# Optimization experiments

Hardware: AMD Instinct MI355X
Metric: run time of the kernel (lower is better)

Reference implementation:

```python
import jax, jax.numpy as jnp
import numpy as np
import math

B, S, H, NH, NKV = 4, 2048, 2048, 16, 8
HD = H // NH           # 128
N_REP = NH // NKV      # 2


def rotate_half(t):
    t1, t2 = jnp.split(t, 2, axis=-1)
    return jnp.concatenate([-t2, t1], axis=-1)


def setup_inputs() -> dict:
    key = jax.random.key(0)
    ks = jax.random.split(key, 6)
    x = jax.random.normal(ks[0], (B, S, H), dtype=jnp.float32)
    # realistic RoPE tables [max_pos, head_dim]
    inv_freq = 1.0 / (10000.0 ** (np.arange(0, HD, 2, dtype=np.float32) / HD))
    t = np.arange(S, dtype=np.float32)
    freqs = np.outer(t, inv_freq)                 # [S, HD/2]
    emb = np.concatenate([freqs, freqs], axis=-1)  # [S, HD]
    cos = jnp.asarray(np.cos(emb), dtype=jnp.float32)
    sin = jnp.asarray(np.sin(emb), dtype=jnp.float32)
    sc = 0.02
    Wq = jax.random.normal(ks[1], (H, NH * HD), dtype=jnp.float32) * sc
    Wk = jax.random.normal(ks[2], (H, NKV * HD), dtype=jnp.float32) * sc
    Wv = jax.random.normal(ks[3], (H, NKV * HD), dtype=jnp.float32) * sc
    Wo = jax.random.normal(ks[4], (NH * HD, H), dtype=jnp.float32) * sc
    return {"x": x, "cos": cos, "sin": sin, "Wq": Wq, "Wk": Wk, "Wv": Wv, "Wo": Wo}


def reference(x, cos, sin, Wq, Wk, Wv, Wo):
    bsz, seq_len, _ = x.shape
    xq = (x @ Wq).reshape(bsz, seq_len, NH, HD)
    xk = (x @ Wk).reshape(bsz, seq_len, NKV, HD)
    xv = (x @ Wv).reshape(bsz, seq_len, NKV, HD)

    # RoPE (past_len = 0, no cache)
    c = cos[:seq_len][None, :, None, :]   # [1,S,1,HD]
    s = sin[:seq_len][None, :, None, :]
    xq = xq * c + rotate_half(xq) * s
    xk = xk * c + rotate_half(xk) * s

    # repeat_kv (GQA): [B,S,NKV,HD] -> [B,S,NH,HD]
    xk = jnp.repeat(xk, N_REP, axis=2)
    xv = jnp.repeat(xv, N_REP, axis=2)

    q = xq.transpose(0, 2, 1, 3)  # [B,NH,S,HD]
    k = xk.transpose(0, 2, 1, 3)
    v = xv.transpose(0, 2, 1, 3)

    scores = jnp.einsum('bhqd,bhkd->bhqk', q, k) / math.sqrt(HD)
    causal = jnp.triu(jnp.full((seq_len, seq_len), -jnp.inf, dtype=scores.dtype), k=1)
    scores = scores + causal[None, None]
    probs = jax.nn.softmax(scores.astype(jnp.float32), axis=-1).astype(q.dtype)
    out = jnp.einsum('bhqk,bhkd->bhqd', probs, v)
    out = out.transpose(0, 2, 1, 3).reshape(bsz, seq_len, NH * HD)
    return out @ Wo
```

## Files before the change

kernel.cpp:

```cpp
#include <hip/hip_runtime.h>
#include <stdint.h>

using bf16   = __bf16;
using bf16x4 = __attribute__((ext_vector_type(4))) __bf16;
using bf16x8 = __attribute__((ext_vector_type(8))) __bf16;
using f32x4  = __attribute__((ext_vector_type(4))) float;

#define DEV_INLINE __device__ __forceinline__

DEV_INLINE void gload16(const void* g, const void* l) {
  __builtin_amdgcn_global_load_lds(
      (const __attribute__((address_space(1))) unsigned int*)(uintptr_t)g,
      (__attribute__((address_space(3))) unsigned int*)(unsigned int)(uintptr_t)l,
      16, 0, 0);
}

DEV_INLINE f32x4 mfma16(bf16x8 a, bf16x8 b, f32x4 c) {
  return __builtin_amdgcn_mfma_f32_16x16x32_bf16(a, b, c, 0, 0, 0);
}

__global__ void cast_f32_bf16(const float4* __restrict__ in, bf16* __restrict__ out, int n4) {
  int i = blockIdx.x * 256 + threadIdx.x;
  if (i >= n4) return;
  float4 v = in[i];
  bf16x4 o = { (bf16)v.x, (bf16)v.y, (bf16)v.z, (bf16)v.w };
  *(bf16x4*)(out + (size_t)i * 4) = o;
}

__global__ void transpose_cast(const float* __restrict__ in, bf16* __restrict__ out,
                               int rows, int cols) {
  __shared__ float tile[32][33];
  int c0 = blockIdx.x * 32, r0 = blockIdx.y * 32;
  int t = threadIdx.x, tc = t & 31, tr = t >> 5;
  for (int i = 0; i < 4; ++i)
    tile[tr + i*8][tc] = in[(size_t)(r0 + tr + i*8) * cols + (c0 + tc)];
  __syncthreads();
  for (int i = 0; i < 4; ++i)
    out[(size_t)(c0 + tr + i*8) * rows + (r0 + tc)] = (bf16)tile[tc][tr + i*8];
}


DEV_INLINE void stage_half(const bf16* __restrict__ src, int K, int k0, bf16* slot,
                           int w, int lr, int lc) {
#pragma unroll
  for (int i = 0; i < 2; ++i)
    gload16(src + (size_t)(w*16 + lr) * K + (k0 + i*32 + lc*8), slot + (w*2 + i) * 512);
}

DEV_INLINE void load_afr(bf16x8 (&af)[4][2], const bf16* slot, int wr2, int l) {
#pragma unroll
  for (int mi = 0; mi < 4; ++mi)
#pragma unroll
    for (int ks = 0; ks < 2; ++ks)
      af[mi][ks] = *(const bf16x8*)(slot + ((wr2*4 + mi)*2 + ks) * 512 + l*8);
}

template<bool PERM>
DEV_INLINE void load_bfr(bf16x8 (&bfr)[2][2], const bf16* slot, int wc2, int l) {
#pragma unroll
  for (int ni = 0; ni < 2; ++ni)
#pragma unroll
    for (int ks = 0; ks < 2; ++ks) {
      int mt = PERM ? (ni*4 + wc2) : (wc2*2 + ni);
      bfr[ni][ks] = *(const bf16x8*)(slot + (mt*2 + ks) * 512 + l*8);
    }
}

DEV_INLINE void mfma_quad(f32x4 (&aq)[4][2], const bf16x8 (&af)[4][2],
                          const bf16x8 (&bfr)[2][2]) {
#pragma unroll
  for (int mi = 0; mi < 4; ++mi)
#pragma unroll
    for (int ni = 0; ni < 2; ++ni)
#pragma unroll
      for (int ks = 0; ks < 2; ++ks)
        aq[mi][ni] = mfma16(af[mi][ks], bfr[ni][ks], aq[mi][ni]);
}

#define WAIT_LGKM0() do { \
  asm volatile("s_waitcnt lgkmcnt(0)" ::: "memory"); \
  __builtin_amdgcn_sched_barrier(0); } while (0)

template<bool PERM, int K, int NK>
DEV_INLINE void gemm256_core(const bf16* __restrict__ A, const bf16* __restrict__ Bt,
                             int bm0, int bn0, bf16* sA, bf16* sB,
                             int w, int l, int lr, int lc, int wr2, int wc2,
                             f32x4 (&acc)[2][2][4][2]) {
  const bf16* Ar0 = A  + (size_t)bm0 * K;
  const bf16* Ar1 = Ar0 + (size_t)128 * K;
  const bf16* Br0 = Bt + (size_t)bn0 * K;
  const bf16* Br1 = Br0 + (size_t)128 * K;
  stage_half(Ar0, K, 0,  sA + 0*8192, w, lr, lc);
  stage_half(Br1, K, 0,  sB + 1*8192, w, lr, lc);
  stage_half(Ar1, K, 0,  sA + 1*8192, w, lr, lc);
  stage_half(Br0, K, 0,  sB + 0*8192, w, lr, lc);
  stage_half(Ar0, K, 64, sA + 2*8192, w, lr, lc);
  stage_half(Br1, K, 64, sB + 3*8192, w, lr, lc);
  __syncthreads();

  for (int kt = 0; kt < NK; ++kt) {
    const int k1 = (kt + 1 < NK ? kt + 1 : 0) * 64;
    const int k2 = (kt + 2 < NK ? kt + 2 : 0) * 64;
    bf16* A0s = sA + ((2*kt    ) & 3) * 8192;
    bf16* A1s = sA + ((2*kt + 1) & 3) * 8192;
    bf16* B0s = sB + ((2*kt    ) & 3) * 8192;
    bf16* B1s = sB + ((2*kt + 1) & 3) * 8192;
    bf16x8 af[4][2], bfr[2][2];

    load_afr(af, A0s, wr2, l);
    load_bfr<PERM>(bfr, B0s, wc2, l);
    stage_half(Ar1, K, k1, sA + ((2*kt + 3) & 3) * 8192, w, lr, lc);
    __builtin_amdgcn_s_barrier();
    WAIT_LGKM0();
    __builtin_amdgcn_s_setprio(1);
    mfma_quad(acc[0][0], af, bfr);
    __builtin_amdgcn_s_setprio(0);
    __builtin_amdgcn_s_barrier();

    load_bfr<PERM>(bfr, B1s, wc2, l);
    stage_half(Br0, K, k1, sB + ((2*kt + 2) & 3) * 8192, w, lr, lc);
    __builtin_amdgcn_s_barrier();
    WAIT_LGKM0();
    __builtin_amdgcn_s_setprio(1);
    mfma_quad(acc[0][1], af, bfr);
    __builtin_amdgcn_s_setprio(0);
    __builtin_amdgcn_s_barrier();

    load_afr(af, A1s, wr2, l);
    stage_half(Ar0, K, k2, sA + ((2*kt + 4) & 3) * 8192, w, lr, lc);
    __builtin_amdgcn_s_barrier();
    WAIT_LGKM0();
    __builtin_amdgcn_s_setprio(1);
    mfma_quad(acc[1][1], af, bfr);
    __builtin_amdgcn_s_setprio(0);
    __builtin_amdgcn_s_barrier();

    load_bfr<PERM>(bfr, B0s, wc2, l);
    stage_half(Br1, K, k2, sB + ((2*kt + 5) & 3) * 8192, w, lr, lc);
    __builtin_amdgcn_s_barrier();
    WAIT_LGKM0();
    __builtin_amdgcn_s_setprio(1);
    mfma_quad(acc[1][0], af, bfr);
    __builtin_amdgcn_s_setprio(0);
    asm volatile("s_waitcnt vmcnt(4)" ::: "memory");
    __builtin_amdgcn_sched_barrier(0);
    __builtin_amdgcn_s_barrier();
  }
  asm volatile("s_waitcnt vmcnt(0)" ::: "memory");
}

__global__ __launch_bounds__(512, 2)
void gemm256_rope(const bf16* __restrict__ A, const bf16* __restrict__ Bt,
                  const float* __restrict__ cs, const float* __restrict__ sn,
                  bf16* __restrict__ Qr, bf16* __restrict__ Kr,
                  bf16* __restrict__ Vbuf) {
  __shared__ bf16 sA[4 * 8192];
  __shared__ bf16 sB[4 * 8192];
  int id = blockIdx.x;
  int swz = (id & 7) * 64 + (id >> 3);
  int tm = swz >> 4, tn = swz & 15;
  int bm0 = tm * 256, bn0 = tn * 256;
  int tid = threadIdx.x, w = tid >> 6, l = tid & 63, lr = l & 15, lc = l >> 4;
  int wr2 = w >> 2, wc2 = w & 3;
  f32x4 acc[2][2][4][2] = {};
  gemm256_core<true, 2048, 32>(A, Bt, bm0, bn0, sA, sB, w, l, lr, lc, wr2, wc2, acc);

  int bb = bm0 >> 11, s0 = bm0 & 2047;
  int dlo = wc2 * 16 + lr;
#pragma unroll
  for (int nh = 0; nh < 2; ++nh) {
    int h128 = tn * 2 + nh;
    if (h128 < 24) {
      const float scale = (h128 < 16) ? 0.08838834764831845f * 1.4426950408889634f : 1.0f;
      bf16* dstB = (h128 < 16)
          ? Qr + (size_t)(bb * 16 + h128) * 2048 * 128
          : Kr + (size_t)(bb * 8 + (h128 - 16)) * 2048 * 128;
#pragma unroll
      for (int mh = 0; mh < 2; ++mh)
#pragma unroll
        for (int mi = 0; mi < 4; ++mi)
#pragma unroll
          for (int r = 0; r < 4; ++r) {
            int sl = s0 + mh*128 + wr2*64 + mi*16 + lc*4 + r;
            float c  = cs[sl * 128 + dlo];
            float sv = sn[sl * 128 + dlo];
            float lo = acc[mh][nh][mi][0][r], hi = acc[mh][nh][mi][1][r];
            bf16* dst = dstB + (size_t)sl * 128 + dlo;
            dst[0]  = (bf16)((lo * c - hi * sv) * scale);
            dst[64] = (bf16)((hi * c + lo * sv) * scale);
          }
    } else {
      int kvh = h128 - 24;
#pragma unroll
      for (int mh = 0; mh < 2; ++mh)
#pragma unroll
        for (int mi = 0; mi < 4; ++mi)
#pragma unroll
          for (int r = 0; r < 4; ++r) {
            int sl = s0 + mh*128 + wr2*64 + mi*16 + lc*4 + r;
            bf16* dst = Vbuf + ((size_t)(bb * 2048) + sl) * 1024 + kvh * 128 + dlo;
            dst[0]  = (bf16)acc[mh][nh][mi][0][r];
            dst[64] = (bf16)acc[mh][nh][mi][1][r];
          }
    }
  }
}

__global__ __launch_bounds__(512, 2)
void gemm256_out(const bf16* __restrict__ A, const bf16* __restrict__ Bt,
                 float* __restrict__ C) {
  __shared__ bf16 sA[4 * 8192];
  __shared__ bf16 sB[4 * 8192];
  int id = blockIdx.x;
  int swz = (id & 7) * 32 + (id >> 3);
  int tm = swz >> 3, tn = swz & 7;
  int bm0 = tm * 256, bn0 = tn * 256;
  int tid = threadIdx.x, w = tid >> 6, l = tid & 63, lr = l & 15, lc = l >> 4;
  int wr2 = w >> 2, wc2 = w & 3;
  f32x4 acc[2][2][4][2] = {};
  gemm256_core<false, 2048, 32>(A, Bt, bm0, bn0, sA, sB, w, l, lr, lc, wr2, wc2, acc);
#pragma unroll
  for (int mh = 0; mh < 2; ++mh)
#pragma unroll
    for (int nh = 0; nh < 2; ++nh)
#pragma unroll
      for (int mi = 0; mi < 4; ++mi)
#pragma unroll
        for (int ni = 0; ni < 2; ++ni)
#pragma unroll
          for (int r = 0; r < 4; ++r) {
            int row = bm0 + mh*128 + wr2*64 + mi*16 + lc*4 + r;
            int col = bn0 + nh*128 + wc2*32 + ni*16 + lr;
            C[(size_t)row * 2048 + col] = acc[mh][nh][mi][ni][r];
          }
}

__global__ void v_transpose(const bf16* __restrict__ Vbuf, bf16* __restrict__ Vt) {
  __shared__ bf16 tile[32][33];
  int s0 = blockIdx.x * 32, d0 = blockIdx.y * 32, bh = blockIdx.z;
  int b = bh >> 3, h = bh & 7;
  int t = threadIdx.x, tc = t & 31, tr = t >> 5;
  for (int i = 0; i < 4; ++i)
    tile[tr + i*8][tc] =
        Vbuf[((size_t)(b*2048) + s0 + tr + i*8) * 1024 + h*128 + d0 + tc];
  __syncthreads();
  for (int i = 0; i < 4; ++i)
    Vt[((size_t)bh * 128 + d0 + tr + i*8) * 2048 + s0 + tc] = tile[tc][tr + i*8];
}

__global__ __launch_bounds__(256, 2)
void attn_kernel(const bf16* __restrict__ Q, const bf16* __restrict__ Kg,
                 const bf16* __restrict__ Vt, bf16* __restrict__ Og) {
  __shared__ bf16 sK[32 * 512];
  __shared__ bf16 sV[32 * 512];
  int qi = 31 - blockIdx.x;
  int bkv = blockIdx.y;
  int b = bkv >> 3, kvh = bkv & 7;
  int tid = threadIdx.x, w = tid >> 6, l = tid & 63, lr = l & 15, lc = l >> 4;
  const bf16* Qb0 = Q + ((size_t)(b*16 + kvh*2) * 2048 + qi*64) * 128;
  const bf16* Qb1 = Qb0 + (size_t)2048 * 128;
  const bf16* Kb  = Kg + (size_t)bkv * 2048 * 128;
  const bf16* Vb  = Vt + (size_t)bkv * 128 * 2048;
  bf16x8 qf0[4], qf1[4];
  for (int ks = 0; ks < 4; ++ks) {
    size_t off = (size_t)(w*16 + lr) * 128 + ks*32 + lc*8;
    qf0[ks] = *(const bf16x8*)(Qb0 + off);
    qf1[ks] = *(const bf16x8*)(Qb1 + off);
  }
  f32x4 o0[8] = {}, o1[8] = {};
  float l0[4] = {0.f,0.f,0.f,0.f}, l1[4] = {0.f,0.f,0.f,0.f};
  int qrow = qi*64 + w*16 + lc*4;
  bf16* sP0 = sK + w * 2048;
  bf16* sP1 = sK + 8192 + w * 2048;
  int tmax = (qi + 2) >> 1;
  for (int t = 0; t < tmax; ++t) {
    __syncthreads();
    for (int i = 0; i < 8; ++i) {
      int id = w*8 + i;
      int nt = id >> 2, ks = id & 3;
      gload16(Kb + (size_t)(t*128 + nt*16 + lr) * 128 + ks*32 + lc*8, sK + id*512);
      gload16(Vb + (size_t)(nt*16 + lr) * 2048 + t*128 + ks*32 + lc*8, sV + id*512);
    }
    __syncthreads();
    f32x4 s0[8] = {}, s1[8] = {};
    for (int nt = 0; nt < 8; ++nt)
      for (int ks = 0; ks < 4; ++ks) {
        bf16x8 kf = *(const bf16x8*)(sK + (nt*4 + ks)*512 + l*8);
        s0[nt] = mfma16(qf0[ks], kf, s0[nt]);
        s1[nt] = mfma16(qf1[ks], kf, s1[nt]);
      }
    if (t == tmax - 1) {
      for (int nt = 0; nt < 8; ++nt) {
        int col = t*128 + nt*16 + lr;
        for (int r = 0; r < 4; ++r)
          if (col > qrow + r) { s0[nt][r] = -1e30f; s1[nt][r] = -1e30f; }
      }
    }
    __syncthreads();
    for (int nt = 0; nt < 8; ++nt) {
      int hi6 = (nt >> 2) * 1024;
      int blk = (nt*2 + (lr >> 3)) & 7;
      int off = lr & 7;
      for (int r = 0; r < 4; ++r) {
        int q = lc*4 + r;
        int addr = hi6 + q*64 + ((blk ^ (q & 7)) * 8) + off;
        float p0 = __builtin_amdgcn_exp2f(s0[nt][r]);
        float p1 = __builtin_amdgcn_exp2f(s1[nt][r]);
        l0[r] += p0;
        l1[r] += p1;
        sP0[addr] = (bf16)p0;
        sP1[addr] = (bf16)p1;
      }
    }
    asm volatile("s_waitcnt lgkmcnt(0)" ::: "memory");
    __builtin_amdgcn_sched_barrier(0);
    bf16x8 pf0[4], pf1[4];
    for (int ks = 0; ks < 4; ++ks) {
      int ra = (ks >> 1)*1024 + lr*64 + ((((ks & 1)*4 + lc) ^ (lr & 7)) * 8);
      pf0[ks] = *(const bf16x8*)(sP0 + ra);
      pf1[ks] = *(const bf16x8*)(sP1 + ra);
    }
    for (int nt = 0; nt < 8; ++nt)
      for (int ks = 0; ks < 4; ++ks) {
        bf16x8 vf = *(const bf16x8*)(sV + (nt*4 + ks)*512 + l*8);
        o0[nt] = mfma16(pf0[ks], vf, o0[nt]);
        o1[nt] = mfma16(pf1[ks], vf, o1[nt]);
      }
  }
  for (int msk = 1; msk < 16; msk <<= 1)
    for (int r = 0; r < 4; ++r) {
      l0[r] += __shfl_xor(l0[r], msk, 64);
      l1[r] += __shfl_xor(l1[r], msk, 64);
    }
  for (int r = 0; r < 4; ++r) {
    float inv0 = 1.f / l0[r];
    float inv1 = 1.f / l1[r];
    size_t row = (size_t)(b*2048) + qi*64 + w*16 + lc*4 + r;
    size_t base0 = row * 2048 + (kvh*2) * 128;
    for (int nt = 0; nt < 8; ++nt) {
      Og[base0 + nt*16 + lr]       = (bf16)(o0[nt][r] * inv0);
      Og[base0 + 128 + nt*16 + lr] = (bf16)(o1[nt][r] * inv1);
    }
  }
}

extern "C" void kernel_launch(void* const* d_in, const int* in_sizes, int n_in,
                              void* d_out, int out_size, void* d_ws, size_t ws_size,
                              hipStream_t stream) {
  (void)in_sizes; (void)n_in; (void)out_size; (void)ws_size;
  const float* x  = (const float*)d_in[0];
  const float* cs = (const float*)d_in[1];
  const float* sn = (const float*)d_in[2];
  const float* Wq = (const float*)d_in[3];
  const float* Wk = (const float*)d_in[4];
  const float* Wv = (const float*)d_in[5];
  const float* Wo = (const float*)d_in[6];
  float* out = (float*)d_out;

  char* p = (char*)d_ws;
  bf16* xb    = (bf16*)p;  p += (size_t)8192*2048*2;
  bf16* Wt    = (bf16*)p;  p += (size_t)4096*2048*2;
  bf16* Wot   = (bf16*)p;  p += (size_t)2048*2048*2;
  bf16* Qr    = (bf16*)p;  p += (size_t)64*2048*128*2;
  bf16* Kr    = (bf16*)p;  p += (size_t)32*2048*128*2;
  bf16* Vbuf  = (bf16*)p;  p += (size_t)8192*1024*2;
  bf16* Vtb   = (bf16*)p;  p += (size_t)32*2048*128*2;
  bf16* attnb = (bf16*)p;  p += (size_t)8192*2048*2;

  cast_f32_bf16<<<4194304/256, 256, 0, stream>>>((const float4*)x, xb, 4194304);
  transpose_cast<<<dim3(64,64), 256, 0, stream>>>(Wq, Wt, 2048, 2048);
  transpose_cast<<<dim3(32,64), 256, 0, stream>>>(Wk, Wt + (size_t)2048*2048, 2048, 1024);
  transpose_cast<<<dim3(32,64), 256, 0, stream>>>(Wv, Wt + (size_t)3072*2048, 2048, 1024);
  transpose_cast<<<dim3(64,64), 256, 0, stream>>>(Wo, Wot, 2048, 2048);
  gemm256_rope<<<dim3(512), 512, 0, stream>>>(xb, Wt, cs, sn, Qr, Kr, Vbuf);
  v_transpose<<<dim3(64,4,32), 256, 0, stream>>>(Vbuf, Vtb);
  attn_kernel<<<dim3(32,32), 256, 0, stream>>>(Qr, Kr, Vtb, attnb);
  gemm256_out<<<dim3(256), 512, 0, stream>>>(attnb, Wot, out);
}
```

Baseline: 560.3 us.

## Double-buffer K/V tiles in attention kernel and rotate query-block mapping

The attention kernel now keeps two LDS buffers for K and V and prefetches the next tile with async global-to-LDS loads while the current tile is computed, waiting on vmcnt instead of a full barrier. This hides global load latency behind the QK and PV MFMAs. Q-block indices are also rotated per batch-head so causal work is spread across the grid rather than running longest blocks first. LDS use doubles, which may lower occupancy, and the last iteration issues a redundant reload.

```diff
diff --git a/kernel.cpp b/kernel.cpp
--- a/kernel.cpp
+++ b/kernel.cpp
@@ -18,6 +18,15 @@
 DEV_INLINE f32x4 mfma16(bf16x8 a, bf16x8 b, f32x4 c) {
   return __builtin_amdgcn_mfma_f32_16x16x32_bf16(a, b, c, 0, 0, 0);
 }
+
+#define FENCED_BARRIER() do { \
+  __builtin_amdgcn_sched_barrier(0); \
+  __builtin_amdgcn_s_barrier(); \
+  __builtin_amdgcn_sched_barrier(0); } while (0)
+
+#define WAIT_LGKM0() do { \
+  asm volatile("s_waitcnt lgkmcnt(0)" ::: "memory"); \
+  __builtin_amdgcn_sched_barrier(0); } while (0)
 
 __global__ void cast_f32_bf16(const float4* __restrict__ in, bf16* __restrict__ out, int n4) {
   int i = blockIdx.x * 256 + threadIdx.x;
@@ -76,10 +85,6 @@
       for (int ks = 0; ks < 2; ++ks)
         aq[mi][ni] = mfma16(af[mi][ks], bfr[ni][ks], aq[mi][ni]);
 }
-
-#define WAIT_LGKM0() do { \
-  asm volatile("s_waitcnt lgkmcnt(0)" ::: "memory"); \
-  __builtin_amdgcn_sched_barrier(0); } while (0)
 
 template<bool PERM, int K, int NK>
 DEV_INLINE void gemm256_core(const bf16* __restrict__ A, const bf16* __restrict__ Bt,
@@ -251,10 +256,11 @@
 __global__ __launch_bounds__(256, 2)
 void attn_kernel(const bf16* __restrict__ Q, const bf16* __restrict__ Kg,
                  const bf16* __restrict__ Vt, bf16* __restrict__ Og) {
-  __shared__ bf16 sK[32 * 512];
-  __shared__ bf16 sV[32 * 512];
-  int qi = 31 - blockIdx.x;
-  int bkv = blockIdx.y;
+  __shared__ bf16 sK[2][32 * 512];
+  __shared__ bf16 sV[2][32 * 512];
+  int x = blockIdx.x, y = blockIdx.y;
+  int qi = (x + y) & 31;
+  int bkv = y;
   int b = bkv >> 3, kvh = bkv & 7;
   int tid = threadIdx.x, w = tid >> 6, l = tid & 63, lr = l & 15, lc = l >> 4;
   const bf16* Qb0 = Q + ((size_t)(b*16 + kvh*2) * 2048 + qi*64) * 128;
@@ -270,22 +276,35 @@
   f32x4 o0[8] = {}, o1[8] = {};
   float l0[4] = {0.f,0.f,0.f,0.f}, l1[4] = {0.f,0.f,0.f,0.f};
   int qrow = qi*64 + w*16 + lc*4;
-  bf16* sP0 = sK + w * 2048;
-  bf16* sP1 = sK + 8192 + w * 2048;
   int tmax = (qi + 2) >> 1;
+
+  for (int i = 0; i < 8; ++i) {
+    int id = w*8 + i;
+    int nt = id >> 2, ks = id & 3;
+    gload16(Kb + (size_t)(nt*16 + lr) * 128 + ks*32 + lc*8, sK[0] + id*512);
+    gload16(Vb + (size_t)(nt*16 + lr) * 2048 + ks*32 + lc*8, sV[0] + id*512);
+  }
+
   for (int t = 0; t < tmax; ++t) {
-    __syncthreads();
+    int cur = t & 1;
+    bf16* sKc = sK[cur];
+    bf16* sVc = sV[cur];
+    FENCED_BARRIER();
+    int tc = (t + 1 < tmax) ? t + 1 : t;
     for (int i = 0; i < 8; ++i) {
       int id = w*8 + i;
       int nt = id >> 2, ks = id & 3;
-      gload16(Kb + (size_t)(t*128 + nt*16 + lr) * 128 + ks*32 + lc*8, sK + id*512);
-      gload16(Vb + (size_t)(nt*16 + lr) * 2048 + t*128 + ks*32 + lc*8, sV + id*512);
-    }
-    __syncthreads();
+      gload16(Kb + (size_t)(tc*128 + nt*16 + lr) * 128 + ks*32 + lc*8,
+              sK[cur ^ 1] + id*512);
+      gload16(Vb + (size_t)(nt*16 + lr) * 2048 + tc*128 + ks*32 + lc*8,
+              sV[cur ^ 1] + id*512);
+    }
+    asm volatile("s_waitcnt vmcnt(16)" ::: "memory");
+    FENCED_BARRIER();
     f32x4 s0[8] = {}, s1[8] = {};
     for (int nt = 0; nt < 8; ++nt)
       for (int ks = 0; ks < 4; ++ks) {
-        bf16x8 kf = *(const bf16x8*)(sK + (nt*4 + ks)*512 + l*8);
+        bf16x8 kf = *(const bf16x8*)(sKc + (nt*4 + ks)*512 + l*8);
         s0[nt] = mfma16(qf0[ks], kf, s0[nt]);
         s1[nt] = mfma16(qf1[ks], kf, s1[nt]);
       }
@@ -296,7 +315,10 @@
           if (col > qrow + r) { s0[nt][r] = -1e30f; s1[nt][r] = -1e30f; }
       }
     }
-    __syncthreads();
+    WAIT_LGKM0();
+    FENCED_BARRIER();
+    bf16* sP0 = sKc + w * 2048;
+    bf16* sP1 = sKc + 8192 + w * 2048;
     for (int nt = 0; nt < 8; ++nt) {
       int hi6 = (nt >> 2) * 1024;
       int blk = (nt*2 + (lr >> 3)) & 7;
@@ -312,8 +334,7 @@
         sP1[addr] = (bf16)p1;
       }
     }
-    asm volatile("s_waitcnt lgkmcnt(0)" ::: "memory");
-    __builtin_amdgcn_sched_barrier(0);
+    WAIT_LGKM0();
     bf16x8 pf0[4], pf1[4];
     for (int ks = 0; ks < 4; ++ks) {
       int ra = (ks >> 1)*1024 + lr*64 + ((((ks & 1)*4 + lc) ^ (lr & 7)) * 8);
@@ -322,11 +343,12 @@
     }
     for (int nt = 0; nt < 8; ++nt)
       for (int ks = 0; ks < 4; ++ks) {
-        bf16x8 vf = *(const bf16x8*)(sV + (nt*4 + ks)*512 + l*8);
+        bf16x8 vf = *(const bf16x8*)(sVc + (nt*4 + ks)*512 + l*8);
         o0[nt] = mfma16(pf0[ks], vf, o0[nt]);
         o1[nt] = mfma16(pf1[ks], vf, o1[nt]);
       }
   }
+  asm volatile("s_waitcnt vmcnt(0)" ::: "memory");
   for (int msk = 1; msk < 16; msk <<= 1)
     for (int r = 0; r < 4; ++r) {
       l0[r] += __shfl_xor(l0[r], msk, 64);
```

Measured after the change: 632.5 us. 12.9% more time.

## Shrink attention KV tile to 64 with dedicated P buffer and higher occupancy

Applied to the files above, without the earlier changes.

The attention kernel now processes 64-key tiles instead of 128, which makes the causal tail finer-grained. It gives P its own shared buffer so the sync before the P writes can be removed, and the smaller LDS footprint allows launch bounds of 3 blocks per CU. Query tiles are assigned through a rotated (x+y)&31 mapping to balance causal work across blocks. The trade-off is more loop iterations and barriers per block, plus tighter register limits at occupancy 3.

```diff
diff --git a/kernel.cpp b/kernel.cpp
--- a/kernel.cpp
+++ b/kernel.cpp
@@ -18,6 +18,10 @@
 DEV_INLINE f32x4 mfma16(bf16x8 a, bf16x8 b, f32x4 c) {
   return __builtin_amdgcn_mfma_f32_16x16x32_bf16(a, b, c, 0, 0, 0);
 }
+
+#define WAIT_LGKM0() do { \
+  asm volatile("s_waitcnt lgkmcnt(0)" ::: "memory"); \
+  __builtin_amdgcn_sched_barrier(0); } while (0)
 
 __global__ void cast_f32_bf16(const float4* __restrict__ in, bf16* __restrict__ out, int n4) {
   int i = blockIdx.x * 256 + threadIdx.x;
@@ -76,10 +80,6 @@
       for (int ks = 0; ks < 2; ++ks)
         aq[mi][ni] = mfma16(af[mi][ks], bfr[ni][ks], aq[mi][ni]);
 }
-
-#define WAIT_LGKM0() do { \
-  asm volatile("s_waitcnt lgkmcnt(0)" ::: "memory"); \
-  __builtin_amdgcn_sched_barrier(0); } while (0)
 
 template<bool PERM, int K, int NK>
 DEV_INLINE void gemm256_core(const bf16* __restrict__ A, const bf16* __restrict__ Bt,
@@ -248,13 +248,15 @@
     Vt[((size_t)bh * 128 + d0 + tr + i*8) * 2048 + s0 + tc] = tile[tc][tr + i*8];
 }
 
-__global__ __launch_bounds__(256, 2)
+__global__ __launch_bounds__(256, 3)
 void attn_kernel(const bf16* __restrict__ Q, const bf16* __restrict__ Kg,
                  const bf16* __restrict__ Vt, bf16* __restrict__ Og) {
-  __shared__ bf16 sK[32 * 512];
-  __shared__ bf16 sV[32 * 512];
-  int qi = 31 - blockIdx.x;
-  int bkv = blockIdx.y;
+  __shared__ bf16 sK[16 * 512];
+  __shared__ bf16 sV[16 * 512];
+  __shared__ bf16 sP[8 * 1024];
+  int x = blockIdx.x, y = blockIdx.y;
+  int qi = (x + y) & 31;
+  int bkv = y;
   int b = bkv >> 3, kvh = bkv & 7;
   int tid = threadIdx.x, w = tid >> 6, l = tid & 63, lr = l & 15, lc = l >> 4;
   const bf16* Qb0 = Q + ((size_t)(b*16 + kvh*2) * 2048 + qi*64) * 128;
@@ -270,40 +272,39 @@
   f32x4 o0[8] = {}, o1[8] = {};
   float l0[4] = {0.f,0.f,0.f,0.f}, l1[4] = {0.f,0.f,0.f,0.f};
   int qrow = qi*64 + w*16 + lc*4;
-  bf16* sP0 = sK + w * 2048;
-  bf16* sP1 = sK + 8192 + w * 2048;
-  int tmax = (qi + 2) >> 1;
+  bf16* sP0 = sP + w * 1024;
+  bf16* sP1 = sP + 4096 + w * 1024;
+  int tmax = qi + 1;
   for (int t = 0; t < tmax; ++t) {
     __syncthreads();
-    for (int i = 0; i < 8; ++i) {
-      int id = w*8 + i;
-      int nt = id >> 2, ks = id & 3;
-      gload16(Kb + (size_t)(t*128 + nt*16 + lr) * 128 + ks*32 + lc*8, sK + id*512);
-      gload16(Vb + (size_t)(nt*16 + lr) * 2048 + t*128 + ks*32 + lc*8, sV + id*512);
+    for (int i = 0; i < 4; ++i) {
+      int id = w*4 + i;
+      int ntk = id >> 2, ksk = id & 3;
+      gload16(Kb + (size_t)(t*64 + ntk*16 + lr) * 128 + ksk*32 + lc*8, sK + id*512);
+      int ntd = id >> 1, ksv = id & 1;
+      gload16(Vb + (size_t)(ntd*16 + lr) * 2048 + t*64 + ksv*32 + lc*8, sV + id*512);
     }
     __syncthreads();
-    f32x4 s0[8] = {}, s1[8] = {};
-    for (int nt = 0; nt < 8; ++nt)
+    f32x4 s0[4] = {}, s1[4] = {};
+    for (int nt = 0; nt < 4; ++nt)
       for (int ks = 0; ks < 4; ++ks) {
         bf16x8 kf = *(const bf16x8*)(sK + (nt*4 + ks)*512 + l*8);
         s0[nt] = mfma16(qf0[ks], kf, s0[nt]);
         s1[nt] = mfma16(qf1[ks], kf, s1[nt]);
       }
     if (t == tmax - 1) {
-      for (int nt = 0; nt < 8; ++nt) {
-        int col = t*128 + nt*16 + lr;
+      for (int nt = 0; nt < 4; ++nt) {
+        int col = t*64 + nt*16 + lr;
         for (int r = 0; r < 4; ++r)
           if (col > qrow + r) { s0[nt][r] = -1e30f; s1[nt][r] = -1e30f; }
       }
     }
-    __syncthreads();
-    for (int nt = 0; nt < 8; ++nt) {
-      int hi6 = (nt >> 2) * 1024;
-      int blk = (nt*2 + (lr >> 3)) & 7;
+    for (int nt = 0; nt < 4; ++nt) {
+      int blk = nt*2 + (lr >> 3);
       int off = lr & 7;
       for (int r = 0; r < 4; ++r) {
         int q = lc*4 + r;
-        int addr = hi6 + q*64 + ((blk ^ (q & 7)) * 8) + off;
+        int addr = q*64 + (((blk ^ q) & 7) * 8) + off;
         float p0 = __builtin_amdgcn_exp2f(s0[nt][r]);
         float p1 = __builtin_amdgcn_exp2f(s1[nt][r]);
         l0[r] += p0;
@@ -312,17 +313,16 @@
         sP1[addr] = (bf16)p1;
       }
     }
-    asm volatile("s_waitcnt lgkmcnt(0)" ::: "memory");
-    __builtin_amdgcn_sched_barrier(0);
-    bf16x8 pf0[4], pf1[4];
-    for (int ks = 0; ks < 4; ++ks) {
-      int ra = (ks >> 1)*1024 + lr*64 + ((((ks & 1)*4 + lc) ^ (lr & 7)) * 8);
+    WAIT_LGKM0();
+    bf16x8 pf0[2], pf1[2];
+    for (int ks = 0; ks < 2; ++ks) {
+      int ra = lr*64 + (((ks*4 + lc) ^ (lr & 7)) * 8);
       pf0[ks] = *(const bf16x8*)(sP0 + ra);
       pf1[ks] = *(const bf16x8*)(sP1 + ra);
     }
     for (int nt = 0; nt < 8; ++nt)
-      for (int ks = 0; ks < 4; ++ks) {
-        bf16x8 vf = *(const bf16x8*)(sV + (nt*4 + ks)*512 + l*8);
+      for (int ks = 0; ks < 2; ++ks) {
+        bf16x8 vf = *(const bf16x8*)(sV + (nt*2 + ks)*512 + l*8);
         o0[nt] = mfma16(pf0[ks], vf, o0[nt]);
         o1[nt] = mfma16(pf1[ks], vf, o1[nt]);
       }
```

Result: slower. 686.1 us (+22.4%).
